# Kernel tuning notes

Measured on AMD Instinct MI355X. Metric: run time of the kernel, lower is better.

## Reference

```python
import jax, jax.numpy as jnp
import numpy as np

B, S, H, W, DF, D, HID, ITERS = 8, 8, 64, 64, 64, 64, 128, 3
EPS = 1e-8


def build_grid(h, w):
    ranges = [np.linspace(-1.0, 1.0, num=h), np.linspace(-1.0, 1.0, num=w)]
    g = np.meshgrid(*ranges, sparse=False, indexing='xy')
    return jnp.asarray(np.stack(g, axis=-1), dtype=jnp.float32)  # [H, W, 2]


def ln(x, g, b):
    m = jnp.mean(x, axis=-1, keepdims=True)
    v = jnp.mean((x - m) ** 2, axis=-1, keepdims=True)
    return (x - m) * jax.lax.rsqrt(v + 1e-5) * g + b


def setup_inputs() -> dict:
    key = jax.random.key(0)
    ks = iter(jax.random.split(key, 64))
    def nrm(shape, s=0.02):
        return jax.random.normal(next(ks), shape, jnp.float32) * s
    inp = {}
    inp['inputs'] = jax.random.normal(next(ks), (B, H, W, DF), jnp.float32)
    # learned slot inits and learned per-slot position / scale factors
    inp['slots_p'] = jax.random.normal(next(ks), (1, S, D), jnp.float32)
    inp['s_pos_p'] = 2.0 * jax.random.uniform(next(ks), (1, S, 2), jnp.float32) - 1.0
    inp['s_scale_p'] = 0.1 + 0.01 * jax.random.normal(next(ks), (1, S, 2), jnp.float32)
    # soft position embedding Linear(2, D)
    inp['W_pos'] = nrm((2, D)); inp['b_pos'] = jnp.zeros((D,), jnp.float32)
    # q/k/v projections
    inp['Wq'] = nrm((D, D)); inp['bq'] = jnp.zeros((D,), jnp.float32)
    inp['Wk'] = nrm((DF, D)); inp['bk'] = jnp.zeros((D,), jnp.float32)
    inp['Wv'] = nrm((DF, D)); inp['bv'] = jnp.zeros((D,), jnp.float32)
    # layernorms
    inp['g_in'] = jnp.ones((DF,), jnp.float32); inp['b_in'] = jnp.zeros((DF,), jnp.float32)
    inp['g_slots'] = jnp.ones((D,), jnp.float32); inp['b_slots'] = jnp.zeros((D,), jnp.float32)
    inp['g_k'] = jnp.ones((D,), jnp.float32); inp['b_k'] = jnp.zeros((D,), jnp.float32)
    inp['g_v'] = jnp.ones((D,), jnp.float32); inp['b_v'] = jnp.zeros((D,), jnp.float32)
    # shared kv MLP fc1_kv / fc2_kv
    inp['W1'] = nrm((D, 2 * D)); inp['b1'] = jnp.zeros((2 * D,), jnp.float32)
    inp['W2'] = nrm((2 * D, D)); inp['b2'] = jnp.zeros((D,), jnp.float32)
    # GRUCell (torch layout transposed to [in, 3*D])
    inp['W_ih'] = nrm((D, 3 * D)); inp['b_ih'] = jnp.zeros((3 * D,), jnp.float32)
    inp['W_hh'] = nrm((D, 3 * D)); inp['b_hh'] = jnp.zeros((3 * D,), jnp.float32)
    # residual slot MLP
    inp['g_pre'] = jnp.ones((D,), jnp.float32); inp['b_pre'] = jnp.zeros((D,), jnp.float32)
    inp['Wf1'] = nrm((D, HID)); inp['bf1'] = jnp.zeros((HID,), jnp.float32)
    inp['Wf2'] = nrm((HID, D)); inp['bf2'] = jnp.zeros((D,), jnp.float32)
    return inp


def reference(inputs, slots_p, s_pos_p, s_scale_p, W_pos, b_pos, Wq, bq, Wk, bk, Wv, bv,
              g_in, b_in, g_slots, b_slots, g_k, b_k, g_v, b_v, W1, b1, W2, b2,
              W_ih, W_hh, b_ih, b_hh, g_pre, b_pre, Wf1, bf1, Wf2, bf2):
    grid = build_grid(H, W)                 # [H, W, 2]
    grid_flat = grid.reshape(-1, 2)          # [HW, 2]
    scale = D ** (-0.5)

    x = ln(inputs, g_in, b_in)
    k0 = x @ Wk + bk                         # [B, H, W, D]
    v0 = x @ Wv + bv

    slots = jnp.broadcast_to(slots_p, (B, S, D))
    s_pos = jnp.clip(jnp.broadcast_to(s_pos_p, (B, S, 2)), -1.0, 1.0)[:, :, None, None, :]
    s_scale = jnp.clip(jnp.broadcast_to(s_scale_p, (B, S, 2)), 1e-3, 2.0)[:, :, None, None, :]

    def proj_kv(base, sp, ss, g, b):
        gr = (grid[None, None] - sp) / (ss * 5.0)      # [B, S, H, W, 2]
        pe = gr @ W_pos + b_pos                        # [B, S, H, W, D]
        t = (base[:, None] + pe).reshape(B, S, H * W, D)
        t = ln(t, g, b)
        return jax.nn.relu(t @ W1 + b1) @ W2 + b2      # [B, S, HW, D]

    for i in range(ITERS + 1):
        slots_prev = slots
        q = ln(slots, g_slots, b_slots) @ Wq + bq       # [B, S, D]
        kk = proj_kv(k0, s_pos, s_scale, g_k, b_k)
        vv = proj_kv(v0, s_pos, s_scale, g_v, b_v)
        dots = jnp.einsum('bid,bijd->bij', q, kk) * scale
        attn_mask = jax.nn.softmax(dots, axis=1) + EPS  # softmax over slot axis
        attn = attn_mask / jnp.sum(attn_mask, axis=-1, keepdims=True)
        updates = jnp.einsum('bijd,bij->bid', vv, attn)
        if i < ITERS:
            xg = updates.reshape(-1, D) @ W_ih + b_ih
            hg = slots_prev.reshape(-1, D) @ W_hh + b_hh
            ir, iz, inn = jnp.split(xg, 3, axis=-1)
            hr, hz, hn = jnp.split(hg, 3, axis=-1)
            r = jax.nn.sigmoid(ir + hr)
            z = jax.nn.sigmoid(iz + hz)
            n = jnp.tanh(inn + r * hn)
            slots = ((1.0 - z) * n + z * slots_prev.reshape(-1, D)).reshape(B, S, D)
            slots = slots + (jax.nn.relu(ln(slots, g_pre, b_pre) @ Wf1 + bf1) @ Wf2 + bf2)
        else:
            slots = slots_prev
        # update per-slot position / scale from the attention mask
        sp = jnp.einsum('bij,jd->bid', attn_mask, grid_flat) / jnp.sum(attn_mask, axis=-1, keepdims=True)
        diff = grid_flat[None, None] - sp[:, :, None]   # [B, S, HW, 2]
        am = attn_mask + 1e-8
        ss = jnp.sqrt(jnp.einsum('bij,bijd->bid', am, diff ** 2) / jnp.sum(am, axis=-1, keepdims=True))
        s_pos = sp[:, :, None, None, :]
        s_scale = jnp.clip(ss, 1e-3, 2.0)[:, :, None, None, :]
    return slots, s_pos, s_scale, attn_mask
```

## Files before the change

### kernel.cpp

```cpp
#include <hip/hip_runtime.h>
#include <math.h>

typedef __bf16 bf16_t;
typedef __bf16 bfrag __attribute__((ext_vector_type(8)));
typedef float ffrag __attribute__((ext_vector_type(4)));

__device__ __forceinline__ float wave_sum(float v) {
#pragma unroll
  for (int m = 32; m >= 1; m >>= 1) v += __shfl_xor(v, m, 64);
  return v;
}
__device__ __forceinline__ float lin_(int i) { return -1.f + (2.f * (float)i) / 63.f; }
__device__ __forceinline__ float bflo(unsigned u) { return __uint_as_float(u << 16); }
__device__ __forceinline__ float bfhi(unsigned u) { return __uint_as_float(u & 0xFFFF0000u); }

__device__ __forceinline__ void pass_type(
    const bf16_t xs[][72], bf16_t t0s[][72],
    const bf16_t WTl[][72], const bf16_t W1l[][72],
    const float* __restrict__ bias, const float* wpxs, const float* wpys,
    const float* bpvs, float* __restrict__ statsG, bf16_t* __restrict__ P0G,
    int j0, int wv, int lq, int ln15) {
  ffrag C[4] = {{0,0,0,0},{0,0,0,0},{0,0,0,0},{0,0,0,0}};
#pragma unroll
  for (int ks = 0; ks < 2; ++ks) {
    bfrag a = *(const bfrag*)&xs[wv * 16 + ln15][ks * 32 + lq * 8];
#pragma unroll
    for (int nt = 0; nt < 4; ++nt) {
      bfrag bb = *(const bfrag*)&WTl[nt * 16 + ln15][ks * 32 + lq * 8];
      C[nt] = __builtin_amdgcn_mfma_f32_16x16x32_bf16(a, bb, C[nt], 0, 0, 0);
    }
  }
  float kv[4][4];
  float st[5][4];
#pragma unroll
  for (int i = 0; i < 5; ++i)
#pragma unroll
    for (int rg = 0; rg < 4; ++rg) st[i][rg] = 0.f;
#pragma unroll
  for (int nt = 0; nt < 4; ++nt) {
    int n = nt * 16 + ln15;
    float bn = bias[n], pxw = wpxs[n], pyw = wpys[n], bpw = bpvs[n];
#pragma unroll
    for (int rg = 0; rg < 4; ++rg) {
      float v = C[nt][rg] + bn;
      kv[nt][rg] = v;
      st[0][rg] += v; st[1][rg] += v * v; st[2][rg] += v * pxw;
      st[3][rg] += v * pyw; st[4][rg] += v * bpw;
    }
  }
#pragma unroll
  for (int i = 0; i < 5; ++i)
#pragma unroll
    for (int rg = 0; rg < 4; ++rg) {
      float v = st[i][rg];
      v += __shfl_xor(v, 1, 64); v += __shfl_xor(v, 2, 64);
      v += __shfl_xor(v, 4, 64); v += __shfl_xor(v, 8, 64);
      st[i][rg] = v;
    }
  if (ln15 == 0) {
#pragma unroll
    for (int rg = 0; rg < 4; ++rg) {
      int j = j0 + wv * 16 + lq * 4 + rg;
#pragma unroll
      for (int i = 0; i < 5; ++i) statsG[(size_t)j * 10 + i] = st[i][rg];
    }
  }
#pragma unroll
  for (int nt = 0; nt < 4; ++nt)
#pragma unroll
    for (int rg = 0; rg < 4; ++rg)
      t0s[wv * 16 + lq * 4 + rg][nt * 16 + ln15] = (bf16_t)kv[nt][rg];
  ffrag D[8] = {{0,0,0,0},{0,0,0,0},{0,0,0,0},{0,0,0,0},
                {0,0,0,0},{0,0,0,0},{0,0,0,0},{0,0,0,0}};
#pragma unroll
  for (int ks = 0; ks < 2; ++ks) {
    bfrag a = *(const bfrag*)&t0s[wv * 16 + ln15][ks * 32 + lq * 8];
#pragma unroll
    for (int nt = 0; nt < 8; ++nt) {
      bfrag bb = *(const bfrag*)&W1l[nt * 16 + ln15][ks * 32 + lq * 8];
      D[nt] = __builtin_amdgcn_mfma_f32_16x16x32_bf16(a, bb, D[nt], 0, 0, 0);
    }
  }
#pragma unroll
  for (int nt = 0; nt < 8; ++nt)
#pragma unroll
    for (int rg = 0; rg < 4; ++rg)
      P0G[(size_t)(j0 + wv * 16 + lq * 4 + rg) * 128 + nt * 16 + ln15] =
          (bf16_t)D[nt][rg];
}

__global__ __launch_bounds__(256) void k_pre(
    const float* __restrict__ inp, const float* __restrict__ g_in,
    const float* __restrict__ b_in, const float* __restrict__ bk,
    const float* __restrict__ bv, const float* __restrict__ Wk,
    const float* __restrict__ Wv, const float* __restrict__ W1,
    const float* __restrict__ g_k, const float* __restrict__ g_v,
    const float* __restrict__ W_pos, const float* __restrict__ b_pos,
    bf16_t* __restrict__ P0k, bf16_t* __restrict__ P0v,
    float* __restrict__ statsC,
    const float* __restrict__ slots_p, const float* __restrict__ g_slots,
    const float* __restrict__ b_slots, const float* __restrict__ Wq,
    const float* __restrict__ bq, const float* __restrict__ W2,
    const float* __restrict__ b2, float* __restrict__ w2qg,
    float* __restrict__ b2qg,
    const float* __restrict__ b_k, const float* __restrict__ b_v,
    const float* __restrict__ b1, const float* __restrict__ s_pos_p,
    const float* __restrict__ s_scale_p,
    float4* __restrict__ nckA, float* __restrict__ nckB,
    float4* __restrict__ ncvA, float* __restrict__ ncvB,
    float* __restrict__ possum, float* __restrict__ sposS,
    float* __restrict__ sscaleS, float* __restrict__ slotsS) {
  __shared__ bf16_t xs[64][72];
  __shared__ bf16_t t0s[64][72];
  __shared__ bf16_t WkTl[64][72];
  __shared__ bf16_t WvTl[64][72];
  __shared__ bf16_t W1kl[128][72];
  __shared__ bf16_t W1vl[128][72];
  __shared__ float wpxs[64], wpys[64], bpvs[64];
  const int tid = threadIdx.x;
  const int j0 = blockIdx.x * 64;
  for (int i = tid; i < 4096; i += 256) {
    int n = i & 63, d = i >> 6;
    WkTl[n][d] = (bf16_t)Wk[i];
    WvTl[n][d] = (bf16_t)Wv[i];
  }
  for (int i = tid; i < 8192; i += 256) {
    int n = i & 127, c = i >> 7;
    float w = W1[i];
    W1kl[n][c] = (bf16_t)(g_k[c] * w);
    W1vl[n][c] = (bf16_t)(g_v[c] * w);
  }
  if (tid < 64) { wpxs[tid] = W_pos[tid]; wpys[tid] = W_pos[64 + tid]; bpvs[tid] = b_pos[tid]; }
  {
    const int px = tid >> 2, cg = tid & 3;
    const float* rowp = inp + (size_t)(j0 + px) * 64 + cg * 16;
    float v[16];
    *(float4*)&v[0]  = ((const float4*)rowp)[0];
    *(float4*)&v[4]  = ((const float4*)rowp)[1];
    *(float4*)&v[8]  = ((const float4*)rowp)[2];
    *(float4*)&v[12] = ((const float4*)rowp)[3];
    float s = 0.f, s2 = 0.f;
#pragma unroll
    for (int i = 0; i < 16; ++i) { s += v[i]; s2 += v[i] * v[i]; }
    s += __shfl_xor(s, 1, 64); s += __shfl_xor(s, 2, 64);
    s2 += __shfl_xor(s2, 1, 64); s2 += __shfl_xor(s2, 2, 64);
    float m = s * 0.015625f;
    float r = rsqrtf(s2 * 0.015625f - m * m + 1e-5f);
    float g[16], bb[16];
    *(float4*)&g[0]  = ((const float4*)(g_in + cg * 16))[0];
    *(float4*)&g[4]  = ((const float4*)(g_in + cg * 16))[1];
    *(float4*)&g[8]  = ((const float4*)(g_in + cg * 16))[2];
    *(float4*)&g[12] = ((const float4*)(g_in + cg * 16))[3];
    *(float4*)&bb[0]  = ((const float4*)(b_in + cg * 16))[0];
    *(float4*)&bb[4]  = ((const float4*)(b_in + cg * 16))[1];
    *(float4*)&bb[8]  = ((const float4*)(b_in + cg * 16))[2];
    *(float4*)&bb[12] = ((const float4*)(b_in + cg * 16))[3];
#pragma unroll
    for (int e = 0; e < 8; ++e) {
      float x0 = (v[2 * e] - m) * r * g[2 * e] + bb[2 * e];
      float x1 = (v[2 * e + 1] - m) * r * g[2 * e + 1] + bb[2 * e + 1];
      union { unsigned u; bf16_t h[2]; } cv;
      cv.h[0] = (bf16_t)x0; cv.h[1] = (bf16_t)x1;
      *(unsigned*)&xs[px][cg * 16 + 2 * e] = cv.u;
    }
  }
  __syncthreads();
  const int wv = tid >> 6, lane = tid & 63, lq = lane >> 4, ln15 = lane & 15;
  pass_type(xs, t0s, WkTl, W1kl, bk, wpxs, wpys, bpvs, statsC, P0k, j0, wv, lq, ln15);
  __syncthreads();
  pass_type(xs, t0s, WvTl, W1vl, bv, wpxs, wpys, bpvs, statsC + 5, P0v, j0, wv, lq, ln15);
  if (blockIdx.x < 64 && tid < 64) {
    int bs = blockIdx.x, d = tid;
    float v = slots_p[(bs & 7) * 64 + d];
    float m = wave_sum(v) * 0.015625f;
    float c = v - m;
    float var = wave_sum(c * c) * 0.015625f;
    float xn = c * rsqrtf(var + 1e-5f) * g_slots[d] + b_slots[d];
    float q = bq[d];
    for (int cc = 0; cc < 64; ++cc) q = fmaf(__shfl(xn, cc, 64), Wq[cc * 64 + d], q);
    float w0 = 0.f, w1 = 0.f;
    for (int cc = 0; cc < 64; ++cc) {
      float qc = __shfl(q, cc, 64);
      w0 = fmaf(W2[d * 64 + cc], qc, w0);
      w1 = fmaf(W2[(64 + d) * 64 + cc], qc, w1);
    }
    w2qg[bs * 128 + d] = w0;
    w2qg[bs * 128 + 64 + d] = w1;
    float p = wave_sum(b2[d] * q);
    if (d == 0) b2qg[bs] = p;
  }
  if (blockIdx.x == 508 && tid < 128) {
    int n = tid;
    float wx = 0, wy = 0, wb = 0, u = 0, sk = 0;
    for (int c = 0; c < 64; ++c) {
      float w = W1[c * 128 + n];
      float wf = g_k[c] * w;
      float px = W_pos[c], py = W_pos[64 + c], bp = b_pos[c];
      wx += px * wf; wy += py * wf; wb += bp * wf; sk += wf; u += b_k[c] * w;
    }
    nckA[n] = make_float4(wx, wy, wb, u + b1[n]); nckB[n] = sk;
  }
  if (blockIdx.x == 509 && tid < 128) {
    int n = tid;
    float wx = 0, wy = 0, wb = 0, u = 0, sv = 0;
    for (int c = 0; c < 64; ++c) {
      float w = W1[c * 128 + n];
      float wf = g_v[c] * w;
      float px = W_pos[c], py = W_pos[64 + c], bp = b_pos[c];
      wx += px * wf; wy += py * wf; wb += bp * wf; sv += wf; u += b_v[c] * w;
    }
    ncvA[n] = make_float4(wx, wy, wb, u + b1[n]); ncvB[n] = sv;
  }
  if (blockIdx.x == 510) {
    if (tid < 64) {
      float px = W_pos[tid], py = W_pos[64 + tid], bp = b_pos[tid];
      float s9[9] = {px, py, bp, px * px, py * py, bp * bp, px * py, px * bp, py * bp};
#pragma unroll
      for (int i = 0; i < 9; ++i) {
        float v = wave_sum(s9[i]);
        if (tid == 0) possum[i] = v;
      }
    }
    if (tid < 128) {
      sposS[tid] = fminf(fmaxf(s_pos_p[tid & 15], -1.f), 1.f);
      sscaleS[tid] = fminf(fmaxf(s_scale_p[tid & 15], 0.001f), 2.f);
    }
    for (int i = tid; i < 4096; i += 256) slotsS[i] = slots_p[i & 511];
  }
}

template <int LAST>
__global__ __launch_bounds__(256, 4) void k_iter(
    const bf16_t* __restrict__ P0kg, const bf16_t* __restrict__ P0vg,
    const float* __restrict__ statsC,
    const float4* __restrict__ nckA, const float* __restrict__ nckB,
    const float4* __restrict__ ncvA, const float* __restrict__ ncvB,
    const float* __restrict__ possum, const float* __restrict__ w2qg,
    const float* __restrict__ b2qg, const float* __restrict__ sposS,
    const float* __restrict__ sscaleS, float* __restrict__ momP,
    float* __restrict__ HsumP, float* __restrict__ outAttn) {
  __shared__ unsigned P0vl[32 * 65];
  __shared__ float ncqT[128 * 16];
  __shared__ float4 scalV[32][9];
  __shared__ float attnS[32][10];
  __shared__ float momAcc[8][5];
  const int tid = threadIdx.x;
  const int L = blockIdx.x + 128 * blockIdx.y;
  const int xcd = L & 7, cc_ = (L >> 3) & 15, b = L >> 7;
  const int tile = 2 * (xcd + 8 * (cc_ >> 1)) + (cc_ & 1);
  const int jg0 = b * 4096 + tile * 32;
  const int px = tid >> 3, sp = tid & 7;
  uint4 pk0 = ((const uint4*)P0kg)[(size_t)(jg0 + px) * 16 + sp * 2 + 0];
  uint4 pk1 = ((const uint4*)P0kg)[(size_t)(jg0 + px) * 16 + sp * 2 + 1];
  float skA[5], svA[5];
  {
    const int lb = (tid & 63) & ~7;
    float sv0 = statsC[(size_t)(jg0 + px) * 10 + sp];
    float sv1 = 0.f;
    if (!LAST && sp < 2) sv1 = statsC[(size_t)(jg0 + px) * 10 + 8 + sp];
#pragma unroll
    for (int i = 0; i < 5; ++i) skA[i] = __shfl(sv0, lb + i, 64);
    if (!LAST) {
      svA[0] = __shfl(sv0, lb + 5, 64);
      svA[1] = __shfl(sv0, lb + 6, 64);
      svA[2] = __shfl(sv0, lb + 7, 64);
      svA[3] = __shfl(sv1, lb + 0, 64);
      svA[4] = __shfl(sv1, lb + 1, 64);
    }
  }
  if (!LAST) {
#pragma unroll
    for (int r = 0; r < 2; ++r) {
      int idx = tid + 256 * r;
      int row = idx >> 4, seg = idx & 15;
      uint4 w = ((const uint4*)P0vg)[(size_t)(jg0 + row) * 16 + seg];
      unsigned* d2 = &P0vl[row * 65 + seg * 4];
      d2[0] = w.x; d2[1] = w.y; d2[2] = w.z; d2[3] = w.w;
    }
  }
  {
    int n = tid & 127, g = tid >> 7, r4 = ((n >> 4) & 3) * 4;
    float* row = &ncqT[n * 16];
    if (g == 0) {
      float4 A = nckA[n];
      row[(0 + r4) & 15] = A.x; row[(1 + r4) & 15] = A.y;
      row[(2 + r4) & 15] = A.z; row[(3 + r4) & 15] = A.w;
#pragma unroll
      for (int s = 0; s < 4; ++s) row[(4 + s + r4) & 15] = w2qg[(b * 8 + s) * 128 + n];
    } else {
#pragma unroll
      for (int s = 4; s < 8; ++s) row[(4 + s + r4) & 15] = w2qg[(b * 8 + s) * 128 + n];
      row[(12 + r4) & 15] = nckB[n];
    }
  }
  if (tid < 40) momAcc[tid / 5][tid % 5] = 0.f;
  __syncthreads();

  const int jimg = tile * 32 + px;
  const float gx = lin_(jimg & 63), gy = lin_(jimg >> 6);
  const float Swx = possum[0], Swy = possum[1], Sbp = possum[2];
  const float Swx2 = possum[3], Swy2 = possum[4], Sbp2 = possum[5];
  const float Swxy = possum[6], Swxb = possum[7], Swyb = possum[8];
  float c1a[8], c2a[8], rKa[8], mrKa[8];
#pragma unroll
  for (int s = 0; s < 8; ++s) {
    int bs = b * 8 + s;
    float spx = sposS[bs * 2], spy = sposS[bs * 2 + 1];
    float rxx = 1.f / (sscaleS[bs * 2] * 5.f);
    float ryy = 1.f / (sscaleS[bs * 2 + 1] * 5.f);
    float c1 = (gx - spx) * rxx, c2 = (gy - spy) * ryy;
    float quad = c1 * c1 * Swx2 + c2 * c2 * Swy2 + Sbp2 +
                 2.f * (c1 * c2 * Swxy + c1 * Swxb + c2 * Swyb);
    float mK = (skA[0] + c1 * Swx + c2 * Swy + Sbp) * 0.015625f;
    float e2K = (skA[1] + 2.f * (c1 * skA[2] + c2 * skA[3] + skA[4]) + quad) * 0.015625f;
    float rK = rsqrtf(e2K - mK * mK + 1e-5f);
    c1a[s] = c1; c2a[s] = c2; rKa[s] = rK; mrKa[s] = mK * rK;
    if (!LAST && s == sp) {
      float mV = (svA[0] + c1 * Swx + c2 * Swy + Sbp) * 0.015625f;
      float e2V = (svA[1] + 2.f * (c1 * svA[2] + c2 * svA[3] + svA[4]) + quad) * 0.015625f;
      float rV = rsqrtf(e2V - mV * mV + 1e-5f);
      scalV[px][s] = make_float4(c1, c2, rV, mV * rV);
    }
  }
  const unsigned uu[8] = {pk0.x, pk0.y, pk0.z, pk0.w, pk1.x, pk1.y, pk1.z, pk1.w};
  const int r4 = (sp & 3) * 4;
  float d8[8] = {0, 0, 0, 0, 0, 0, 0, 0};
#pragma unroll
  for (int i = 0; i < 8; ++i) {
    int n0 = 16 * sp + 2 * i;
    const float* R0 = &ncqT[n0 * 16];
    const float* R1 = R0 + 16;
    float4 A0 = *(const float4*)&R0[r4];
    float4 q0a = *(const float4*)&R0[(r4 + 4) & 15];
    float4 q0b = *(const float4*)&R0[(r4 + 8) & 15];
    float ws0 = R0[(r4 + 12) & 15];
    float4 A1 = *(const float4*)&R1[r4];
    float4 q1a = *(const float4*)&R1[(r4 + 4) & 15];
    float4 q1b = *(const float4*)&R1[(r4 + 8) & 15];
    float ws1 = R1[(r4 + 12) & 15];
    float qq0[8] = {q0a.x, q0a.y, q0a.z, q0a.w, q0b.x, q0b.y, q0b.z, q0b.w};
    float qq1[8] = {q1a.x, q1a.y, q1a.z, q1a.w, q1b.x, q1b.y, q1b.z, q1b.w};
    float p0 = bflo(uu[i]), p1 = bfhi(uu[i]);
    float bm0 = p0 + A0.z, bm1 = p1 + A1.z;
#pragma unroll
    for (int s = 0; s < 8; ++s) {
      float z0 = bm0 + c1a[s] * A0.x + c2a[s] * A0.y;
      float h0 = fmaxf(fmaf(rKa[s], z0, fmaf(-mrKa[s], ws0, A0.w)), 0.f);
      d8[s] = fmaf(h0, qq0[s], d8[s]);
      float z1 = bm1 + c1a[s] * A1.x + c2a[s] * A1.y;
      float h1 = fmaxf(fmaf(rKa[s], z1, fmaf(-mrKa[s], ws1, A1.w)), 0.f);
      d8[s] = fmaf(h1, qq1[s], d8[s]);
    }
  }
#pragma unroll
  for (int s = 0; s < 8; ++s) {
    float v = d8[s];
    v += __shfl_xor(v, 1, 64);
    v += __shfl_xor(v, 2, 64);
    v += __shfl_xor(v, 4, 64);
    d8[s] = (v + b2qg[b * 8 + s]) * 0.125f;
  }
  float mx = d8[0];
#pragma unroll
  for (int s = 1; s < 8; ++s) mx = fmaxf(mx, d8[s]);
  float tt = 0.f;
  float e8[8];
#pragma unroll
  for (int s = 0; s < 8; ++s) { e8[s] = expf(d8[s] - mx); tt += e8[s]; }
  float inv = 1.f / tt;
#pragma unroll
  for (int s = 0; s < 8; ++s) e8[s] = e8[s] * inv + 1e-8f;
  attnS[px][sp] = e8[sp];
  if (LAST) outAttn[(size_t)(b * 8 + sp) * 4096 + jimg] = e8[sp];
  {
    float w = e8[sp];
    float mm[5] = {w, w * gx, w * gy, w * gx * gx, w * gy * gy};
#pragma unroll
    for (int i = 0; i < 5; ++i) {
      float v = mm[i];
      v += __shfl_xor(v, 8, 64); v += __shfl_xor(v, 16, 64);
      v += __shfl_xor(v, 32, 64);
      mm[i] = v;
    }
    if ((tid & 63) < 8) {
#pragma unroll
      for (int i = 0; i < 5; ++i) atomicAdd(&momAcc[sp][i], mm[i]);
    }
  }
  __syncthreads();
  if (tid < 40)
    momP[((size_t)(b * 8 + tid / 5) * 128 + tile) * 5 + tid % 5] =
        momAcc[tid / 5][tid % 5];

  if (!LAST) {
    const int w = tid >> 6, l = tid & 63;
    const int s0 = 2 * w, s1 = 2 * w + 1;
    float4 cv0 = ncvA[2 * l], cv1 = ncvA[2 * l + 1];
    float wv0 = ncvB[2 * l], wv1 = ncvB[2 * l + 1];
    float h00 = 0.f, h01 = 0.f, h10 = 0.f, h11 = 0.f;
#pragma unroll 4
    for (int j = 0; j < 32; ++j) {
      unsigned u = P0vl[j * 65 + l];
      float pv0 = bflo(u), pv1 = bfhi(u);
      float bm0 = pv0 + cv0.z, bm1 = pv1 + cv1.z;
      float4 sa = scalV[j][s0]; float aw = attnS[j][s0];
      float z0 = bm0 + sa.x * cv0.x + sa.y * cv0.y;
      h00 = fmaf(aw, fmaxf(fmaf(sa.z, z0, fmaf(-sa.w, wv0, cv0.w)), 0.f), h00);
      float z1 = bm1 + sa.x * cv1.x + sa.y * cv1.y;
      h01 = fmaf(aw, fmaxf(fmaf(sa.z, z1, fmaf(-sa.w, wv1, cv1.w)), 0.f), h01);
      float4 sb = scalV[j][s1]; float ab = attnS[j][s1];
      float z2 = bm0 + sb.x * cv0.x + sb.y * cv0.y;
      h10 = fmaf(ab, fmaxf(fmaf(sb.z, z2, fmaf(-sb.w, wv0, cv0.w)), 0.f), h10);
      float z3 = bm1 + sb.x * cv1.x + sb.y * cv1.y;
      h11 = fmaf(ab, fmaxf(fmaf(sb.z, z3, fmaf(-sb.w, wv1, cv1.w)), 0.f), h11);
    }
    *(float2*)&HsumP[((size_t)(b * 8 + s0) * 128 + tile) * 128 + 2 * l] =
        make_float2(h00, h01);
    *(float2*)&HsumP[((size_t)(b * 8 + s1) * 128 + tile) * 128 + 2 * l] =
        make_float2(h10, h11);
  }
}

__global__ __launch_bounds__(192) void k_fin(
    const float* __restrict__ momP, const float* __restrict__ HsumP,
    const float* __restrict__ W2, const float* __restrict__ b2,
    const float* __restrict__ W_ih, const float* __restrict__ b_ih,
    const float* __restrict__ W_hh, const float* __restrict__ b_hh,
    const float* __restrict__ g_pre, const float* __restrict__ b_pre,
    const float* __restrict__ Wf1, const float* __restrict__ bf1,
    const float* __restrict__ Wf2, const float* __restrict__ bf2,
    const float* __restrict__ g_slots, const float* __restrict__ b_slots,
    const float* __restrict__ Wq, const float* __restrict__ bq,
    float* __restrict__ slotsS, float* __restrict__ sposS, float* __restrict__ sscaleS,
    float* __restrict__ w2qg, float* __restrict__ b2qg,
    float* __restrict__ outSlots, float* __restrict__ outSpos,
    float* __restrict__ outSscale, int last) {
  const int bs = blockIdx.x;
  const int t = threadIdx.x;
  __shared__ float hsum_s[128], upd[64], sprev[64], xg[192], hg[192];
  __shared__ float snew[64], xpre[64], hf[128], sfin[64], xn[64], qsh[64];
  __shared__ float mom_s[5];
  if (t < 64) {
    const float* mp = momP + ((size_t)bs * 128 + t) * 5;
    float m0 = mp[0] + mp[320], m1 = mp[1] + mp[321], m2 = mp[2] + mp[322];
    float m3 = mp[3] + mp[323], m4 = mp[4] + mp[324];
    m0 = wave_sum(m0); m1 = wave_sum(m1); m2 = wave_sum(m2);
    m3 = wave_sum(m3); m4 = wave_sum(m4);
    if (t == 0) { mom_s[0] = m0; mom_s[1] = m1; mom_s[2] = m2; mom_s[3] = m3; mom_s[4] = m4; }
    if (!last) sprev[t] = slotsS[bs * 64 + t];
  }
  if (!last && t >= 64) {
    int n = t - 64;
    const float* hp = HsumP + (size_t)bs * 16384 + n;
    float a = 0.f;
#pragma unroll 8
    for (int tile = 0; tile < 128; ++tile) a += hp[tile * 128];
    hsum_s[n] = a;
  }
  __syncthreads();
  const float M0 = mom_s[0];
  const float M1x = mom_s[1], M1y = mom_s[2];
  const float M2x = mom_s[3], M2y = mom_s[4];
  const float invM0 = 1.f / M0;
  const float spx = M1x * invM0, spy = M1y * invM0;
  const float M0a = M0 + 4096.f * 1e-8f;
  const float G2 = 1408.6772487f * 1e-8f;
  const float vx = (M2x + G2 - 2.f * spx * M1x + spx * spx * M0a) / M0a;
  const float vy = (M2y + G2 - 2.f * spy * M1y + spy * spy * M0a) / M0a;
  float ssx = sqrtf(fmaxf(vx, 0.f)), ssy = sqrtf(fmaxf(vy, 0.f));
  ssx = fminf(fmaxf(ssx, 0.001f), 2.f);
  ssy = fminf(fmaxf(ssy, 0.001f), 2.f);
  if (t == 0) {
    sposS[bs * 2 + 0] = spx; sposS[bs * 2 + 1] = spy;
    sscaleS[bs * 2 + 0] = ssx; sscaleS[bs * 2 + 1] = ssy;
    if (last) {
      outSpos[bs * 2 + 0] = spx; outSpos[bs * 2 + 1] = spy;
      outSscale[bs * 2 + 0] = ssx; outSscale[bs * 2 + 1] = ssy;
    }
  }
  if (last) {
    if (t < 64) outSlots[bs * 64 + t] = slotsS[bs * 64 + t];
    return;
  }
  if (t < 64) {
    float a = 0.f;
#pragma unroll
    for (int k = 0; k < 128; ++k) a += hsum_s[k] * W2[k * 64 + t];
    upd[t] = a * invM0 + b2[t];
  }
  __syncthreads();
  {
    float a = b_ih[t], h = b_hh[t];
#pragma unroll
    for (int d = 0; d < 64; ++d) {
      a += upd[d] * W_ih[d * 192 + t];
      h += sprev[d] * W_hh[d * 192 + t];
    }
    xg[t] = a; hg[t] = h;
  }
  __syncthreads();
  if (t < 64) {
    float r = 1.f / (1.f + expf(-(xg[t] + hg[t])));
    float z = 1.f / (1.f + expf(-(xg[64 + t] + hg[64 + t])));
    float n = tanhf(xg[128 + t] + r * hg[128 + t]);
    snew[t] = (1.f - z) * n + z * sprev[t];
  }
  __syncthreads();
  if (t < 64) {
    float v = snew[t];
    float m = wave_sum(v) * 0.015625f;
    float c = v - m;
    float var = wave_sum(c * c) * 0.015625f;
    xpre[t] = c * rsqrtf(var + 1e-5f) * g_pre[t] + b_pre[t];
  }
  __syncthreads();
  if (t < 128) {
    float a = bf1[t];
#pragma unroll
    for (int d = 0; d < 64; ++d) a += xpre[d] * Wf1[d * 128 + t];
    hf[t] = fmaxf(a, 0.f);
  }
  __syncthreads();
  if (t < 64) {
    float a = bf2[t];
#pragma unroll
    for (int k = 0; k < 128; ++k) a += hf[k] * Wf2[k * 64 + t];
    float nv = snew[t] + a;
    slotsS[bs * 64 + t] = nv;
    sfin[t] = nv;
  }
  __syncthreads();
  if (t < 64) {
    float v = sfin[t];
    float m = wave_sum(v) * 0.015625f;
    float c = v - m;
    float var = wave_sum(c * c) * 0.015625f;
    xn[t] = c * rsqrtf(var + 1e-5f) * g_slots[t] + b_slots[t];
  }
  __syncthreads();
  if (t < 64) {
    float a = bq[t];
#pragma unroll
    for (int d = 0; d < 64; ++d) a += xn[d] * Wq[d * 64 + t];
    qsh[t] = a;
  }
  __syncthreads();
  if (t < 128) {
    float a = 0.f;
#pragma unroll
    for (int d = 0; d < 64; ++d) a += W2[t * 64 + d] * qsh[d];
    w2qg[bs * 128 + t] = a;
  }
  if (t < 64) {
    float p = wave_sum(b2[t] * qsh[t]);
    if (t == 0) b2qg[bs] = p;
  }
}

extern "C" void kernel_launch(void* const* d_in, const int* in_sizes, int n_in,
                              void* d_out, int out_size, void* d_ws, size_t ws_size,
                              hipStream_t stream) {
  (void)in_sizes; (void)n_in; (void)out_size; (void)ws_size;
  const float* const* in = (const float* const*)d_in;
  float* ws = (float*)d_ws;
  bf16_t* P0k   = (bf16_t*)(ws + 0);
  bf16_t* P0v   = (bf16_t*)(ws + 2097152);
  float* statsC = ws + 4194304;
  float* w2qg   = ws + 4521984;
  float* b2qg   = ws + 4530176;
  float* slotsS = ws + 4530240;
  float* sposS  = ws + 4534336;
  float* sscaleS= ws + 4534464;
  float4* nckA  = (float4*)(ws + 4555392);
  float* nckB   = ws + 4555904;
  float4* ncvA  = (float4*)(ws + 4556032);
  float* ncvB   = ws + 4556544;
  float* possum = ws + 4556672;
  float* HsumP  = ws + 4560896;
  float* momP   = ws + 5609472;

  float* out = (float*)d_out;
  float* outSlots  = out;
  float* outSpos   = out + 4096;
  float* outSscale = out + 4224;
  float* outAttn   = out + 4352;

  k_pre<<<512, 256, 0, stream>>>(
      in[0], in[12], in[13], in[9], in[11], in[8], in[10], in[20], in[16], in[18],
      in[4], in[5], P0k, P0v, statsC,
      in[1], in[14], in[15], in[6], in[7], in[22], in[23], w2qg, b2qg,
      in[17], in[19], in[21], in[2], in[3],
      nckA, nckB, ncvA, ncvB, possum, sposS, sscaleS, slotsS);
  for (int i = 0; i < 4; ++i) {
    int last = (i == 3) ? 1 : 0;
    if (!last) {
      k_iter<0><<<dim3(128, 8), 256, 0, stream>>>(
          P0k, P0v, statsC, nckA, nckB, ncvA, ncvB, possum,
          w2qg, b2qg, sposS, sscaleS, momP, HsumP, outAttn);
    } else {
      k_iter<1><<<dim3(128, 8), 256, 0, stream>>>(
          P0k, P0v, statsC, nckA, nckB, ncvA, ncvB, possum,
          w2qg, b2qg, sposS, sscaleS, momP, HsumP, outAttn);
    }
    k_fin<<<64, 192, 0, stream>>>(momP, HsumP, in[22], in[23], in[24], in[25],
                                  in[26], in[27], in[28], in[29], in[30], in[31],
                                  in[32], in[33], in[14], in[15], in[6], in[7],
                                  slotsS, sposS, sscaleS, w2qg, b2qg,
                                  outSlots, outSpos, outSscale, last);
  }
}
```

Before: 268.0 us.

## Fuse first attention iteration into preprocessing kernel using LDS-resident projections

Merges the first k_iter pass into the preprocessing kernel. Each block keeps its 64 pixels' projected K/V features and stats in LDS and runs the slot attention, moments and value-hidden accumulation directly, so it neither re-reads them from global memory nor pays one kernel launch. Global stores of P0 now go through an LDS staging buffer as coalesced 16-byte writes. In exchange every block redundantly recomputes the small per-slot and weight-folded constants, and uses about 74 KB of LDS per block, which may lower occupancy.

```diff
diff --git a/kernel.cpp b/kernel.cpp
--- a/kernel.cpp
+++ b/kernel.cpp
@@ -14,12 +14,13 @@
 __device__ __forceinline__ float bflo(unsigned u) { return __uint_as_float(u << 16); }
 __device__ __forceinline__ float bfhi(unsigned u) { return __uint_as_float(u & 0xFFFF0000u); }
 
-__device__ __forceinline__ void pass_type(
-    const bf16_t xs[][72], bf16_t t0s[][72],
-    const bf16_t WTl[][72], const bf16_t W1l[][72],
+__device__ __forceinline__ void pass_fused(
+    const bf16_t (*xs)[72], bf16_t (*t0s)[72],
+    const bf16_t (*WTl)[72], const bf16_t (*W1l)[72],
     const float* __restrict__ bias, const float* wpxs, const float* wpys,
-    const float* bpvs, float* __restrict__ statsG, bf16_t* __restrict__ P0G,
-    int j0, int wv, int lq, int ln15) {
+    const float* bpvs, float* __restrict__ statsG, float* scrL,
+    unsigned* stg, bf16_t* __restrict__ P0G,
+    int j0, int wv, int lq, int ln15, int tid) {
   ffrag C[4] = {{0,0,0,0},{0,0,0,0},{0,0,0,0},{0,0,0,0}};
 #pragma unroll
   for (int ks = 0; ks < 2; ++ks) {
@@ -81,15 +82,33 @@
       D[nt] = __builtin_amdgcn_mfma_f32_16x16x32_bf16(a, bb, D[nt], 0, 0, 0);
     }
   }
+  __syncthreads();
+  bf16_t* S16 = (bf16_t*)stg;
 #pragma unroll
   for (int nt = 0; nt < 8; ++nt)
 #pragma unroll
     for (int rg = 0; rg < 4; ++rg)
-      P0G[(size_t)(j0 + wv * 16 + lq * 4 + rg) * 128 + nt * 16 + ln15] =
-          (bf16_t)D[nt][rg];
+      S16[(wv * 16 + lq * 4 + rg) * 130 + nt * 16 + ln15] = (bf16_t)D[nt][rg];
+  if (ln15 == 0) {
+#pragma unroll
+    for (int rg = 0; rg < 4; ++rg) {
+      int row = wv * 16 + lq * 4 + rg;
+#pragma unroll
+      for (int i = 0; i < 5; ++i) scrL[row * 10 + i] = st[i][rg];
+    }
+  }
+  __syncthreads();
+#pragma unroll
+  for (int r = 0; r < 4; ++r) {
+    int idx = tid + 256 * r;
+    int row = idx >> 4, seg = idx & 15;
+    const unsigned* sp = &stg[row * 65 + seg * 4];
+    uint4 v = {sp[0], sp[1], sp[2], sp[3]};
+    ((uint4*)P0G)[(size_t)(j0 + row) * 16 + seg] = v;
+  }
 }
 
-__global__ __launch_bounds__(256) void k_pre(
+__global__ __launch_bounds__(256) void k_preit(
     const float* __restrict__ inp, const float* __restrict__ g_in,
     const float* __restrict__ b_in, const float* __restrict__ bk,
     const float* __restrict__ bv, const float* __restrict__ Wk,
@@ -109,15 +128,35 @@
     float4* __restrict__ nckA, float* __restrict__ nckB,
     float4* __restrict__ ncvA, float* __restrict__ ncvB,
     float* __restrict__ possum, float* __restrict__ sposS,
-    float* __restrict__ sscaleS, float* __restrict__ slotsS) {
-  __shared__ bf16_t xs[64][72];
-  __shared__ bf16_t t0s[64][72];
-  __shared__ bf16_t WkTl[64][72];
-  __shared__ bf16_t WvTl[64][72];
-  __shared__ bf16_t W1kl[128][72];
-  __shared__ bf16_t W1vl[128][72];
-  __shared__ float wpxs[64], wpys[64], bpvs[64];
+    float* __restrict__ sscaleS, float* __restrict__ slotsS,
+    float* __restrict__ momP, float* __restrict__ HsumP) {
+  __shared__ __align__(16) char smem[74496];
+  bf16_t (*xs)[72]   = (bf16_t(*)[72])(smem + 27648);
+  bf16_t (*t0s)[72]  = (bf16_t(*)[72])(smem + 36864);
+  bf16_t (*WkTl)[72] = (bf16_t(*)[72])(smem + 0);
+  bf16_t (*W1kl)[72] = (bf16_t(*)[72])(smem + 9216);
+  bf16_t (*WvTl)[72] = (bf16_t(*)[72])(smem + 46080);
+  bf16_t (*W1vl)[72] = (bf16_t(*)[72])(smem + 55296);
+  unsigned* P0klL = (unsigned*)(smem + 0);
+  unsigned* P0vlL = (unsigned*)(smem + 46080);
+  float* scrL  = (float*)(smem + 16640);
+  float* ncqTL = (float*)(smem + 27648);
+  float4 (*scalVL)[9] = (float4(*)[9])(smem + 36864);
+  float (*attnSL)[10] = (float(*)[10])(smem + 41472);
+  float (*momAccL)[5] = (float(*)[5])(smem + 42752);
+  float* ncvAl = (float*)(smem + 62720);
+  float* ncvBl = (float*)(smem + 64768);
+  float (*w2qsL)[128] = (float(*)[128])(smem + 65280);
+  float* b2qsL = (float*)(smem + 69376);
+  float* possL = (float*)(smem + 69440);
+  float* sposL = (float*)(smem + 69504);
+  float* ssclL = (float*)(smem + 69568);
+  float* wpxs = (float*)(smem + 73728);
+  float* wpys = (float*)(smem + 73984);
+  float* bpvs = (float*)(smem + 74240);
+
   const int tid = threadIdx.x;
+  const int batch = blockIdx.x >> 6, tileo = blockIdx.x & 63;
   const int j0 = blockIdx.x * 64;
   for (int i = tid; i < 4096; i += 256) {
     int n = i & 63, d = i >> 6;
@@ -132,8 +171,8 @@
   }
   if (tid < 64) { wpxs[tid] = W_pos[tid]; wpys[tid] = W_pos[64 + tid]; bpvs[tid] = b_pos[tid]; }
   {
-    const int px = tid >> 2, cg = tid & 3;
-    const float* rowp = inp + (size_t)(j0 + px) * 64 + cg * 16;
+    const int pxl = tid >> 2, cg = tid & 3;
+    const float* rowp = inp + (size_t)(j0 + pxl) * 64 + cg * 16;
     float v[16];
     *(float4*)&v[0]  = ((const float4*)rowp)[0];
     *(float4*)&v[4]  = ((const float4*)rowp)[1];
@@ -161,71 +200,238 @@
       float x1 = (v[2 * e + 1] - m) * r * g[2 * e + 1] + bb[2 * e + 1];
       union { unsigned u; bf16_t h[2]; } cv;
       cv.h[0] = (bf16_t)x0; cv.h[1] = (bf16_t)x1;
-      *(unsigned*)&xs[px][cg * 16 + 2 * e] = cv.u;
+      *(unsigned*)&xs[pxl][cg * 16 + 2 * e] = cv.u;
     }
   }
   __syncthreads();
   const int wv = tid >> 6, lane = tid & 63, lq = lane >> 4, ln15 = lane & 15;
-  pass_type(xs, t0s, WkTl, W1kl, bk, wpxs, wpys, bpvs, statsC, P0k, j0, wv, lq, ln15);
-  __syncthreads();
-  pass_type(xs, t0s, WvTl, W1vl, bv, wpxs, wpys, bpvs, statsC + 5, P0v, j0, wv, lq, ln15);
-  if (blockIdx.x < 64 && tid < 64) {
-    int bs = blockIdx.x, d = tid;
-    float v = slots_p[(bs & 7) * 64 + d];
+  pass_fused(xs, t0s, WkTl, W1kl, bk, wpxs, wpys, bpvs, statsC, scrL,
+             P0klL, P0k, j0, wv, lq, ln15, tid);
+  __syncthreads();
+  pass_fused(xs, t0s, WvTl, W1vl, bv, wpxs, wpys, bpvs, statsC + 5, scrL + 5,
+             P0vlL, P0v, j0, wv, lq, ln15, tid);
+  __syncthreads();
+
+  if (tid < 128) {
+    int n = tid;
+    float wx = 0, wy = 0, wb = 0, u = 0, sk = 0;
+    for (int c = 0; c < 64; ++c) {
+      float w = W1[c * 128 + n];
+      float wf = g_k[c] * w;
+      float pxc = W_pos[c], pyc = W_pos[64 + c], bpc = b_pos[c];
+      wx += pxc * wf; wy += pyc * wf; wb += bpc * wf; sk += wf; u += b_k[c] * w;
+    }
+    float4 A = make_float4(wx, wy, wb, u + b1[n]);
+    int rr = ((n >> 4) & 3) * 4;
+    float* row = &ncqTL[n * 16];
+    row[(0 + rr) & 15] = A.x; row[(1 + rr) & 15] = A.y;
+    row[(2 + rr) & 15] = A.z; row[(3 + rr) & 15] = A.w;
+    row[(12 + rr) & 15] = sk;
+    if (blockIdx.x == 0) { nckA[n] = A; nckB[n] = sk; }
+  } else {
+    int n = tid - 128;
+    float wx = 0, wy = 0, wb = 0, u = 0, sv = 0;
+    for (int c = 0; c < 64; ++c) {
+      float w = W1[c * 128 + n];
+      float wf = g_v[c] * w;
+      float pxc = W_pos[c], pyc = W_pos[64 + c], bpc = b_pos[c];
+      wx += pxc * wf; wy += pyc * wf; wb += bpc * wf; sv += wf; u += b_v[c] * w;
+    }
+    ncvAl[n * 4 + 0] = wx; ncvAl[n * 4 + 1] = wy;
+    ncvAl[n * 4 + 2] = wb; ncvAl[n * 4 + 3] = u + b1[n];
+    ncvBl[n] = sv;
+    if (blockIdx.x == 0) { ncvA[n] = make_float4(wx, wy, wb, u + b1[n]); ncvB[n] = sv; }
+  }
+  for (int ss = 0; ss < 2; ++ss) {
+    int s = 2 * wv + ss, d = lane;
+    float v = slots_p[s * 64 + d];
     float m = wave_sum(v) * 0.015625f;
     float c = v - m;
     float var = wave_sum(c * c) * 0.015625f;
-    float xn = c * rsqrtf(var + 1e-5f) * g_slots[d] + b_slots[d];
+    float xnv = c * rsqrtf(var + 1e-5f) * g_slots[d] + b_slots[d];
     float q = bq[d];
-    for (int cc = 0; cc < 64; ++cc) q = fmaf(__shfl(xn, cc, 64), Wq[cc * 64 + d], q);
+    for (int cc = 0; cc < 64; ++cc) q = fmaf(__shfl(xnv, cc, 64), Wq[cc * 64 + d], q);
     float w0 = 0.f, w1 = 0.f;
     for (int cc = 0; cc < 64; ++cc) {
       float qc = __shfl(q, cc, 64);
       w0 = fmaf(W2[d * 64 + cc], qc, w0);
       w1 = fmaf(W2[(64 + d) * 64 + cc], qc, w1);
     }
-    w2qg[bs * 128 + d] = w0;
-    w2qg[bs * 128 + 64 + d] = w1;
+    w2qsL[s][d] = w0;
+    w2qsL[s][64 + d] = w1;
     float p = wave_sum(b2[d] * q);
-    if (d == 0) b2qg[bs] = p;
-  }
-  if (blockIdx.x == 508 && tid < 128) {
-    int n = tid;
-    float wx = 0, wy = 0, wb = 0, u = 0, sk = 0;
-    for (int c = 0; c < 64; ++c) {
-      float w = W1[c * 128 + n];
-      float wf = g_k[c] * w;
-      float px = W_pos[c], py = W_pos[64 + c], bp = b_pos[c];
-      wx += px * wf; wy += py * wf; wb += bp * wf; sk += wf; u += b_k[c] * w;
-    }
-    nckA[n] = make_float4(wx, wy, wb, u + b1[n]); nckB[n] = sk;
-  }
-  if (blockIdx.x == 509 && tid < 128) {
-    int n = tid;
-    float wx = 0, wy = 0, wb = 0, u = 0, sv = 0;
-    for (int c = 0; c < 64; ++c) {
-      float w = W1[c * 128 + n];
-      float wf = g_v[c] * w;
-      float px = W_pos[c], py = W_pos[64 + c], bp = b_pos[c];
-      wx += px * wf; wy += py * wf; wb += bp * wf; sv += wf; u += b_v[c] * w;
-    }
-    ncvA[n] = make_float4(wx, wy, wb, u + b1[n]); ncvB[n] = sv;
-  }
-  if (blockIdx.x == 510) {
-    if (tid < 64) {
-      float px = W_pos[tid], py = W_pos[64 + tid], bp = b_pos[tid];
-      float s9[9] = {px, py, bp, px * px, py * py, bp * bp, px * py, px * bp, py * bp};
-#pragma unroll
-      for (int i = 0; i < 9; ++i) {
-        float v = wave_sum(s9[i]);
-        if (tid == 0) possum[i] = v;
+    if (d == 0) b2qsL[s] = p;
+  }
+  if (tid < 64) {
+    float pxc = wpxs[tid], pyc = wpys[tid], bpc = bpvs[tid];
+    float s9[9] = {pxc, pyc, bpc, pxc * pxc, pyc * pyc, bpc * bpc,
+                   pxc * pyc, pxc * bpc, pyc * bpc};
+#pragma unroll
+    for (int i = 0; i < 9; ++i) {
+      float v = wave_sum(s9[i]);
+      if (tid == 0) { possL[i] = v; if (blockIdx.x == 0) possum[i] = v; }
+    }
+  }
+  if (tid < 16) {
+    sposL[tid] = fminf(fmaxf(s_pos_p[tid], -1.f), 1.f);
+    ssclL[tid] = fminf(fmaxf(s_scale_p[tid], 0.001f), 2.f);
+  }
+  __syncthreads();
+  {
+    int n = tid & 127, g = tid >> 7, rr = ((n >> 4) & 3) * 4;
+    float* row = &ncqTL[n * 16];
+    if (g == 0) {
+#pragma unroll
+      for (int s = 0; s < 4; ++s) row[(4 + s + rr) & 15] = w2qsL[s][n];
+    } else {
+#pragma unroll
+      for (int s = 4; s < 8; ++s) row[(4 + s + rr) & 15] = w2qsL[s][n];
+    }
+  }
+  if (tileo == 0) {
+    for (int i = tid; i < 1024; i += 256) w2qg[batch * 1024 + i] = (&w2qsL[0][0])[i];
+    if (tid < 8) b2qg[batch * 8 + tid] = b2qsL[tid];
+    if (tid < 16) { sposS[batch * 16 + tid] = sposL[tid]; sscaleS[batch * 16 + tid] = ssclL[tid]; }
+    for (int i = tid; i < 512; i += 256) slotsS[batch * 512 + i] = slots_p[i];
+  }
+  __syncthreads();
+  const int l2 = tid & 63, w2 = tid >> 6;
+  float4 cv0 = *(float4*)&ncvAl[(2 * l2) * 4], cv1 = *(float4*)&ncvAl[(2 * l2 + 1) * 4];
+  float wv0 = ncvBl[2 * l2], wv1 = ncvBl[2 * l2 + 1];
+  const float Swx = possL[0], Swy = possL[1], Sbp = possL[2];
+  const float Swx2 = possL[3], Swy2 = possL[4], Sbp2 = possL[5];
+  const float Swxy = possL[6], Swxb = possL[7], Swyb = possL[8];
+  const int px = tid >> 3, sp = tid & 7;
+
+  for (int u = 0; u < 2; ++u) {
+    const int tile = 2 * tileo + u;
+    const int row = u * 32 + px;
+    if (tid < 40) momAccL[tid / 5][tid % 5] = 0.f;
+    __syncthreads();
+    const int jimg = tile * 32 + px;
+    const float gx = lin_(jimg & 63), gy = lin_(jimg >> 6);
+    unsigned uu[8];
+#pragma unroll
+    for (int w = 0; w < 8; ++w) uu[w] = P0klL[row * 65 + sp * 8 + w];
+    float skA[5], svA[5];
+#pragma unroll
+    for (int i = 0; i < 5; ++i) {
+      skA[i] = scrL[row * 10 + i];
+      svA[i] = scrL[row * 10 + 5 + i];
+    }
+    float c1a[8], c2a[8], rKa[8], mrKa[8];
+#pragma unroll
+    for (int s = 0; s < 8; ++s) {
+      float spx = sposL[s * 2], spy = sposL[s * 2 + 1];
+      float rxx = 1.f / (ssclL[s * 2] * 5.f);
+      float ryy = 1.f / (ssclL[s * 2 + 1] * 5.f);
+      float c1 = (gx - spx) * rxx, c2 = (gy - spy) * ryy;
+      float quad = c1 * c1 * Swx2 + c2 * c2 * Swy2 + Sbp2 +
+                   2.f * (c1 * c2 * Swxy + c1 * Swxb + c2 * Swyb);
+      float mK = (skA[0] + c1 * Swx + c2 * Swy + Sbp) * 0.015625f;
+      float e2K = (skA[1] + 2.f * (c1 * skA[2] + c2 * skA[3] + skA[4]) + quad) * 0.015625f;
+      float rK = rsqrtf(e2K - mK * mK + 1e-5f);
+      c1a[s] = c1; c2a[s] = c2; rKa[s] = rK; mrKa[s] = mK * rK;
+      if (s == sp) {
+        float mV = (svA[0] + c1 * Swx + c2 * Swy + Sbp) * 0.015625f;
+        float e2V = (svA[1] + 2.f * (c1 * svA[2] + c2 * svA[3] + svA[4]) + quad) * 0.015625f;
+        float rV = rsqrtf(e2V - mV * mV + 1e-5f);
+        scalVL[px][s] = make_float4(c1, c2, rV, mV * rV);
       }
     }
-    if (tid < 128) {
-      sposS[tid] = fminf(fmaxf(s_pos_p[tid & 15], -1.f), 1.f);
-      sscaleS[tid] = fminf(fmaxf(s_scale_p[tid & 15], 0.001f), 2.f);
-    }
-    for (int i = tid; i < 4096; i += 256) slotsS[i] = slots_p[i & 511];
+    const int rr = (sp & 3) * 4;
+    float d8[8] = {0, 0, 0, 0, 0, 0, 0, 0};
+#pragma unroll
+    for (int i = 0; i < 8; ++i) {
+      int n0 = 16 * sp + 2 * i;
+      const float* R0 = &ncqTL[n0 * 16];
+      const float* R1 = R0 + 16;
+      float4 A0 = *(const float4*)&R0[rr];
+      float4 q0a = *(const float4*)&R0[(rr + 4) & 15];
+      float4 q0b = *(const float4*)&R0[(rr + 8) & 15];
+      float ws0 = R0[(rr + 12) & 15];
+      float4 A1 = *(const float4*)&R1[rr];
+      float4 q1a = *(const float4*)&R1[(rr + 4) & 15];
+      float4 q1b = *(const float4*)&R1[(rr + 8) & 15];
+      float ws1 = R1[(rr + 12) & 15];
+      float qq0[8] = {q0a.x, q0a.y, q0a.z, q0a.w, q0b.x, q0b.y, q0b.z, q0b.w};
+      float qq1[8] = {q1a.x, q1a.y, q1a.z, q1a.w, q1b.x, q1b.y, q1b.z, q1b.w};
+      float p0 = bflo(uu[i]), p1 = bfhi(uu[i]);
+      float bm0 = p0 + A0.z, bm1 = p1 + A1.z;
+#pragma unroll
+      for (int s = 0; s < 8; ++s) {
+        float z0 = bm0 + c1a[s] * A0.x + c2a[s] * A0.y;
+        float h0 = fmaxf(fmaf(rKa[s], z0, fmaf(-mrKa[s], ws0, A0.w)), 0.f);
+        d8[s] = fmaf(h0, qq0[s], d8[s]);
+        float z1 = bm1 + c1a[s] * A1.x + c2a[s] * A1.y;
+        float h1 = fmaxf(fmaf(rKa[s], z1, fmaf(-mrKa[s], ws1, A1.w)), 0.f);
+        d8[s] = fmaf(h1, qq1[s], d8[s]);
+      }
+    }
+#pragma unroll
+    for (int s = 0; s < 8; ++s) {
+      float v = d8[s];
+      v += __shfl_xor(v, 1, 64);
+      v += __shfl_xor(v, 2, 64);
+      v += __shfl_xor(v, 4, 64);
+      d8[s] = (v + b2qsL[s]) * 0.125f;
+    }
+    float mx = d8[0];
+#pragma unroll
+    for (int s = 1; s < 8; ++s) mx = fmaxf(mx, d8[s]);
+    float tt = 0.f;
+    float e8[8];
+#pragma unroll
+    for (int s = 0; s < 8; ++s) { e8[s] = expf(d8[s] - mx); tt += e8[s]; }
+    float inv = 1.f / tt;
+#pragma unroll
+    for (int s = 0; s < 8; ++s) e8[s] = e8[s] * inv + 1e-8f;
+    attnSL[px][sp] = e8[sp];
+    {
+      float w = e8[sp];
+      float mm[5] = {w, w * gx, w * gy, w * gx * gx, w * gy * gy};
+#pragma unroll
+      for (int i = 0; i < 5; ++i) {
+        float v = mm[i];
+        v += __shfl_xor(v, 8, 64); v += __shfl_xor(v, 16, 64);
+        v += __shfl_xor(v, 32, 64);
+        mm[i] = v;
+      }
+      if ((tid & 63) < 8) {
+#pragma unroll
+        for (int i = 0; i < 5; ++i) atomicAdd(&momAccL[sp][i], mm[i]);
+      }
+    }
+    __syncthreads();
+    if (tid < 40)
+      momP[((size_t)(batch * 8 + tid / 5) * 128 + tile) * 5 + tid % 5] =
+          momAccL[tid / 5][tid % 5];
+    {
+      const int s0 = 2 * w2, s1 = 2 * w2 + 1;
+      float h00 = 0.f, h01 = 0.f, h10 = 0.f, h11 = 0.f;
+#pragma unroll 4
+      for (int j = 0; j < 32; ++j) {
+        unsigned uvv = P0vlL[(u * 32 + j) * 65 + l2];
+        float pv0 = bflo(uvv), pv1 = bfhi(uvv);
+        float bm0 = pv0 + cv0.z, bm1 = pv1 + cv1.z;
+        float4 sa = scalVL[j][s0];
+        float4 sb = scalVL[j][s1];
+        float2 awp = *(const float2*)&attnSL[j][s0];
+        float z0 = bm0 + sa.x * cv0.x + sa.y * cv0.y;
+        h00 = fmaf(awp.x, fmaxf(fmaf(sa.z, z0, fmaf(-sa.w, wv0, cv0.w)), 0.f), h00);
+        float z1 = bm1 + sa.x * cv1.x + sa.y * cv1.y;
+        h01 = fmaf(awp.x, fmaxf(fmaf(sa.z, z1, fmaf(-sa.w, wv1, cv1.w)), 0.f), h01);
+        float z2 = bm0 + sb.x * cv0.x + sb.y * cv0.y;
+        h10 = fmaf(awp.y, fmaxf(fmaf(sb.z, z2, fmaf(-sb.w, wv0, cv0.w)), 0.f), h10);
+        float z3 = bm1 + sb.x * cv1.x + sb.y * cv1.y;
+        h11 = fmaf(awp.y, fmaxf(fmaf(sb.z, z3, fmaf(-sb.w, wv1, cv1.w)), 0.f), h11);
+      }
+      *(float2*)&HsumP[((size_t)(batch * 8 + s0) * 128 + tile) * 128 + 2 * l2] =
+          make_float2(h00, h01);
+      *(float2*)&HsumP[((size_t)(batch * 8 + s1) * 128 + tile) * 128 + 2 * l2] =
+          make_float2(h10, h11);
+    }
+    __syncthreads();
   }
 }
 
@@ -295,7 +501,6 @@
   }
   if (tid < 40) momAcc[tid / 5][tid % 5] = 0.f;
   __syncthreads();
-
   const int jimg = tile * 32 + px;
   const float gx = lin_(jimg & 63), gy = lin_(jimg >> 6);
   const float Swx = possum[0], Swy = possum[1], Sbp = possum[2];
@@ -391,7 +596,6 @@
   if (tid < 40)
     momP[((size_t)(b * 8 + tid / 5) * 128 + tile) * 5 + tid % 5] =
         momAcc[tid / 5][tid % 5];
-
   if (!LAST) {
     const int w = tid >> 6, l = tid & 63;
     const int s0 = 2 * w, s1 = 2 * w + 1;
@@ -585,13 +789,19 @@
   float* outSscale = out + 4224;
   float* outAttn   = out + 4352;
 
-  k_pre<<<512, 256, 0, stream>>>(
+  k_preit<<<512, 256, 0, stream>>>(
       in[0], in[12], in[13], in[9], in[11], in[8], in[10], in[20], in[16], in[18],
       in[4], in[5], P0k, P0v, statsC,
       in[1], in[14], in[15], in[6], in[7], in[22], in[23], w2qg, b2qg,
       in[17], in[19], in[21], in[2], in[3],
-      nckA, nckB, ncvA, ncvB, possum, sposS, sscaleS, slotsS);
-  for (int i = 0; i < 4; ++i) {
+      nckA, nckB, ncvA, ncvB, possum, sposS, sscaleS, slotsS,
+      momP, HsumP);
+  k_fin<<<64, 192, 0, stream>>>(momP, HsumP, in[22], in[23], in[24], in[25],
+                                in[26], in[27], in[28], in[29], in[30], in[31],
+                                in[32], in[33], in[14], in[15], in[6], in[7],
+                                slotsS, sposS, sscaleS, w2qg, b2qg,
+                                outSlots, outSpos, outSscale, 0);
+  for (int i = 1; i < 4; ++i) {
     int last = (i == 3) ? 1 : 0;
     if (!last) {
       k_iter<0><<<dim3(128, 8), 256, 0, stream>>>(
```

Result: slower. 288.4 us (+7.6%).
